# Kernel optimization log

Hardware: AMD Instinct MI355X
Metric: run time of the kernel (lower is better)

The kernel has to match this reference:

```python
import jax, jax.numpy as jnp
import numpy as np

B, C, H = 128, 3, 224
PATCH_NUM, PS = 14, 16          # patch_size = image_size / patch_num
NP = PATCH_NUM * PATCH_NUM      # 196 patches
TOP_K = 20
D = 768                         # ViT-B hidden dim
NUM_CLASSES = 1000


def setup_inputs() -> dict:
    key = jax.random.key(0)
    k1, k2, k3, k4, k5 = jax.random.split(key, 5)
    return {
        "inputs": jax.random.normal(k1, (B, C, H, H), jnp.float32),
        "patch_grad": jax.random.normal(k2, (B, NP, D), jnp.float32),
        "attack_w": jax.random.uniform(k3, (C, H, H), jnp.float32),  # torch.rand init
        "w_cls": jax.random.normal(k4, (C * NP, NUM_CLASSES), jnp.float32) * 0.02,
        "targets": jax.random.randint(k5, (B,), 0, NUM_CLASSES),
    }


def reference(inputs, patch_grad, attack_w, w_cls, targets):
    # --- top-k patch selection from patch-embedding gradients ---
    # sum over batch, then over embedding dim -> [NP]
    sum_patch = patch_grad.sum(axis=0).sum(axis=1)
    _, top_idx = jax.lax.top_k(sum_patch, TOP_K)  # distinct patch indices

    # --- vectorized equivalent of the per-pixel double loop ---
    # patch (ix, iy) -> pixel block [ix*PS:(ix+1)*PS, iy*PS:(iy+1)*PS]
    ix = top_idx // PATCH_NUM
    iy = top_idx % PATCH_NUM
    mask_p = jnp.zeros((PATCH_NUM, PATCH_NUM), inputs.dtype).at[ix, iy].set(1.0)
    mask = jnp.kron(mask_p, jnp.ones((PS, PS), inputs.dtype))  # [H, H] pixel mask
    x = inputs + mask[None, None, :, :] * attack_w[None, :, :, :]  # [B,C,H,H]

    # --- surrogate classifier head (stand-in for aux_vit second forward) ---
    # per-patch average pool, flatten, linear -> logits [B, NUM_CLASSES]
    pooled = x.reshape(B, C, PATCH_NUM, PS, PATCH_NUM, PS).mean(axis=(3, 5))
    logits = pooled.reshape(B, -1) @ w_cls

    targets_prob = jax.nn.softmax(logits, axis=1)
    # original applies CrossEntropyLoss to the *probabilities* (treats them as logits)
    logp = jax.nn.log_softmax(targets_prob, axis=1)
    ce = -jnp.take_along_axis(logp, targets[:, None], axis=1)[:, 0]  # [B]

    u = 0.0
    l2loss = jnp.mean(attack_w * attack_w)
    loss = u * l2loss - (1.0 - u) * ce.mean()
    return targets_prob, loss
```

## Files before the change

### kernel.cpp

```cpp
#include <hip/hip_runtime.h>
#include <math.h>

#define PA_OFF    0
#define APOOL_OFF 25600
#define MA_OFF    26624
#define IPOOL_OFF 28672
#define PL_OFF    106496

typedef float v4f __attribute__((ext_vector_type(4)));

__device__ __forceinline__ float hsum4(v4f v) { return (v.x + v.y) + (v.z + v.w); }

__global__ __launch_bounds__(256, 2) void k1_main(
    const float* __restrict__ inputs,
    const float* __restrict__ patch_grad,
    const float* __restrict__ attack_w,
    float* __restrict__ ws)
{
  const int bid  = blockIdx.x;
  const int lane = threadIdx.x & 63;

  if (bid < 784) {
    const int w  = bid * 4 + (threadIdx.x >> 6);
    const int R0 = w * 8;
    const v4f* src = (const v4f*)patch_grad + (size_t)R0 * 192 + lane;

    v4f v[24];
    #pragma unroll
    for (int j = 0; j < 24; ++j)
      v[j] = __builtin_nontemporal_load(src + (size_t)j * 64);
    __builtin_amdgcn_sched_barrier(0);

    float s[8];
    #pragma unroll
    for (int k = 0; k < 8; ++k)
      s[k] = hsum4(v[3 * k]) + hsum4(v[3 * k + 1]) + hsum4(v[3 * k + 2]);

    #pragma unroll
    for (int o = 32; o > 0; o >>= 1) {
      #pragma unroll
      for (int k = 0; k < 8; ++k) s[k] += __shfl_down(s[k], o, 64);
    }
    if (lane == 0) {
      float* pa = ws + PA_OFF;
      #pragma unroll
      for (int k = 0; k < 8; ++k) {
        const int row = R0 + k, b = row / 196, p = row - b * 196;
        pa[p * 128 + b] = s[k];
      }
    }
  } else {
    const int w = (bid - 784) * 4 + (threadIdx.x >> 6);
    if (w >= 5418) return;
    const int img = w / 14, px = w - img * 14;
    const float* base = (img < 384)
        ? inputs + (size_t)img * 50176
        : attack_w + (size_t)(img - 384) * 50176;
    const v4f* src = (const v4f*)(base + px * 3584);
    const int cl = (lane < 56) ? lane : 55;

    v4f v[16];
    #pragma unroll
    for (int r = 0; r < 16; ++r)
      v[r] = __builtin_nontemporal_load(src + r * 56 + cl);
    __builtin_amdgcn_sched_barrier(0);

    v4f s = v[0];
    #pragma unroll
    for (int r = 1; r < 16; ++r) s += v[r];
    s.x += __shfl_xor(s.x, 1); s.y += __shfl_xor(s.y, 1);
    s.z += __shfl_xor(s.z, 1); s.w += __shfl_xor(s.w, 1);
    s.x += __shfl_xor(s.x, 2); s.y += __shfl_xor(s.y, 2);
    s.z += __shfl_xor(s.z, 2); s.w += __shfl_xor(s.w, 2);
    if ((lane & 3) == 0 && lane < 56) {
      const int py = lane >> 2;
      const float ps = ((s.x + s.y) + (s.z + s.w)) * (1.f / 256.f);
      if (img < 384) {
        const int b = img / 3, c = img - b * 3;
        ws[IPOOL_OFF + (size_t)b * 588 + c * 196 + px * 14 + py] = ps;
      } else {
        ws[APOOL_OFF + (img - 384) * 196 + px * 14 + py] = ps;
      }
    }
  }
}

__global__ __launch_bounds__(256) void k2_topk(float* __restrict__ ws,
                                               float* __restrict__ d_loss)
{
  __shared__ float sp[196];
  __shared__ float maskp[196];
  const int t = threadIdx.x;
  if (t < 196) {
    const float4* q = (const float4*)(ws + PA_OFF + (size_t)t * 128);
    float4 a = make_float4(0.f, 0.f, 0.f, 0.f);
    #pragma unroll
    for (int j = 0; j < 32; ++j) {
      const float4 v = q[j];
      a.x += v.x; a.y += v.y; a.z += v.z; a.w += v.w;
    }
    sp[t] = (a.x + a.y) + (a.z + a.w);
  }
  if (t == 0) *d_loss = 0.f;
  __syncthreads();
  if (t < 196) {
    const float v = sp[t];
    int cnt = 0;
    for (int j = 0; j < 196; ++j) {
      const float u = sp[j];
      cnt += (u > v || (u == v && j < t)) ? 1 : 0;
    }
    maskp[t] = (cnt < 20) ? 1.f : 0.f;
  }
  __syncthreads();
  for (int k = t; k < 588; k += 256) {
    const int p = k % 196;
    ws[MA_OFF + k] = maskp[p] * ws[APOOL_OFF + k];
  }
}

__global__ __launch_bounds__(256) void k3_gemm(const float* __restrict__ w_cls,
                                               float* __restrict__ ws)
{
  __shared__ __align__(16) float lp[588 * 8];
  const int bid = blockIdx.x;
  const int nt = bid & 15;
  const int bg = bid >> 4;
  const int t  = threadIdx.x;
  const float* ipool = ws + IPOOL_OFF;
  const float* ma    = ws + MA_OFF;
  for (int idx = t; idx < 4704; idx += 256) {
    const int bb = idx / 588;
    const int kk = idx - bb * 588;
    lp[kk * 8 + bb] = ipool[(size_t)(bg * 8 + bb) * 588 + kk] + ma[kk];
  }
  __syncthreads();
  const int lane = t & 63, g = t >> 6;
  const int n = nt * 64 + lane;
  const bool valid = n < 1000;
  float a0 = 0, a1 = 0;
  const float* wc = w_cls + n;
  #pragma unroll 7
  for (int kk = 0; kk < 588; ++kk) {
    const float w = valid ? wc[(size_t)kk * 1000] : 0.f;
    const float2 pv = *(const float2*)&lp[kk * 8 + g * 2];
    a0 += pv.x * w; a1 += pv.y * w;
  }
  float* pl = ws + PL_OFF;
  const int rowb = bg * 8 + g * 2;
  pl[(size_t)(rowb + 0) * 1024 + n] = a0;
  pl[(size_t)(rowb + 1) * 1024 + n] = a1;
}

__global__ __launch_bounds__(256) void k4_softmax(const float* __restrict__ ws,
                                                  const int* __restrict__ targets,
                                                  float* __restrict__ out)
{
  __shared__ float red[4];
  __shared__ float sh_pt;
  const int b = blockIdx.x, t = threadIdx.x;
  const float* pl = ws + PL_OFF + (size_t)b * 1024;
  float l[4]; bool val[4];
  #pragma unroll
  for (int j = 0; j < 4; ++j) {
    const int n = j * 256 + t;
    val[j] = (n < 1000);
    l[j] = val[j] ? pl[n] : -INFINITY;
  }
  float m = fmaxf(fmaxf(l[0], l[1]), fmaxf(l[2], l[3]));
  #pragma unroll
  for (int o = 32; o > 0; o >>= 1) m = fmaxf(m, __shfl_down(m, o, 64));
  if ((t & 63) == 0) red[t >> 6] = m;
  __syncthreads();
  const float m1 = fmaxf(fmaxf(red[0], red[1]), fmaxf(red[2], red[3]));
  __syncthreads();
  float e[4]; float s = 0.f;
  #pragma unroll
  for (int j = 0; j < 4; ++j) { e[j] = val[j] ? expf(l[j] - m1) : 0.f; s += e[j]; }
  #pragma unroll
  for (int o = 32; o > 0; o >>= 1) s += __shfl_down(s, o, 64);
  if ((t & 63) == 0) red[t >> 6] = s;
  __syncthreads();
  const float S1 = red[0] + red[1] + red[2] + red[3];
  __syncthreads();
  const float inv = 1.f / S1;
  const int tgt = targets[b];
  float p[4];
  #pragma unroll
  for (int j = 0; j < 4; ++j) {
    const int n = j * 256 + t;
    if (val[j]) {
      p[j] = e[j] * inv;
      out[(size_t)b * 1000 + n] = p[j];
      if (n == tgt) sh_pt = p[j];
    } else {
      p[j] = -INFINITY;
    }
  }
  float m2 = fmaxf(fmaxf(p[0], p[1]), fmaxf(p[2], p[3]));
  #pragma unroll
  for (int o = 32; o > 0; o >>= 1) m2 = fmaxf(m2, __shfl_down(m2, o, 64));
  if ((t & 63) == 0) red[t >> 6] = m2;
  __syncthreads();
  const float M2 = fmaxf(fmaxf(red[0], red[1]), fmaxf(red[2], red[3]));
  __syncthreads();
  float s2 = 0.f;
  #pragma unroll
  for (int j = 0; j < 4; ++j) s2 += val[j] ? expf(p[j] - M2) : 0.f;
  #pragma unroll
  for (int o = 32; o > 0; o >>= 1) s2 += __shfl_down(s2, o, 64);
  if ((t & 63) == 0) red[t >> 6] = s2;
  __syncthreads();
  if (t == 0) {
    const float S2 = red[0] + red[1] + red[2] + red[3];
    const float lse2 = M2 + logf(S2);
    atomicAdd(out + 128000, (sh_pt - lse2) * (1.f / 128.f));
  }
}

extern "C" void kernel_launch(void* const* d_in, const int* in_sizes, int n_in,
                              void* d_out, int out_size, void* d_ws, size_t ws_size,
                              hipStream_t stream) {
  const float* inputs     = (const float*)d_in[0];
  const float* patch_grad = (const float*)d_in[1];
  const float* attack_w   = (const float*)d_in[2];
  const float* w_cls      = (const float*)d_in[3];
  const int*   targets    = (const int*)d_in[4];
  float* out = (float*)d_out;
  float* ws  = (float*)d_ws;

  hipLaunchKernelGGL(k1_main,  dim3(2139), dim3(256), 0, stream,
                     inputs, patch_grad, attack_w, ws);
  hipLaunchKernelGGL(k2_topk,  dim3(1),    dim3(256), 0, stream, ws, out + 128000);
  hipLaunchKernelGGL(k3_gemm,  dim3(256),  dim3(256), 0, stream, w_cls, ws);
  hipLaunchKernelGGL(k4_softmax, dim3(128), dim3(256), 0, stream, ws, targets, out);
}
```

Baseline: 235.7 us.

## Split classifier GEMM along K into eight partial slices reduced in softmax

The small GEMM kernel is split along the 588-long reduction dimension into 8 slices, raising the grid from 256 to 2048 blocks so more CUs are busy. Each block writes partial logits to a separate workspace slab, and the softmax kernel sums the 8 partials before proceeding. The padded shared-memory row stride also changes to 9 to reduce bank conflicts. In exchange, the workspace needs 8x more partial-logit storage, there is extra global traffic for the partials, and each block repeats the staging setup.

```diff
diff --git a/kernel.cpp b/kernel.cpp
--- a/kernel.cpp
+++ b/kernel.cpp
@@ -122,34 +122,39 @@
 __global__ __launch_bounds__(256) void k3_gemm(const float* __restrict__ w_cls,
                                                float* __restrict__ ws)
 {
-  __shared__ __align__(16) float lp[588 * 8];
+  __shared__ __align__(16) float lp[74 * 9];
   const int bid = blockIdx.x;
-  const int nt = bid & 15;
-  const int bg = bid >> 4;
+  const int ks = bid & 7;
+  const int nt = (bid >> 3) & 15;
+  const int bg = bid >> 7;
   const int t  = threadIdx.x;
+  const int kk_max = (ks == 7) ? 70 : 74;
   const float* ipool = ws + IPOOL_OFF;
   const float* ma    = ws + MA_OFF;
-  for (int idx = t; idx < 4704; idx += 256) {
-    const int bb = idx / 588;
-    const int kk = idx - bb * 588;
-    lp[kk * 8 + bb] = ipool[(size_t)(bg * 8 + bb) * 588 + kk] + ma[kk];
+  for (int idx = t; idx < 592; idx += 256) {
+    const int bb = idx & 7;
+    const int kk = idx >> 3;
+    const int k  = ks * 74 + kk;
+    lp[kk * 9 + bb] = (kk < kk_max)
+        ? ipool[(size_t)(bg * 8 + bb) * 588 + k] + ma[k]
+        : 0.f;
   }
   __syncthreads();
   const int lane = t & 63, g = t >> 6;
   const int n = nt * 64 + lane;
   const bool valid = n < 1000;
   float a0 = 0, a1 = 0;
-  const float* wc = w_cls + n;
-  #pragma unroll 7
-  for (int kk = 0; kk < 588; ++kk) {
+  const float* wc = w_cls + (size_t)ks * 74 * 1000 + n;
+  #pragma unroll 10
+  for (int kk = 0; kk < kk_max; ++kk) {
     const float w = valid ? wc[(size_t)kk * 1000] : 0.f;
-    const float2 pv = *(const float2*)&lp[kk * 8 + g * 2];
+    const float2 pv = *(const float2*)&lp[kk * 9 + g * 2];
     a0 += pv.x * w; a1 += pv.y * w;
   }
   float* pl = ws + PL_OFF;
   const int rowb = bg * 8 + g * 2;
-  pl[(size_t)(rowb + 0) * 1024 + n] = a0;
-  pl[(size_t)(rowb + 1) * 1024 + n] = a1;
+  pl[(size_t)(ks * 128 + rowb + 0) * 1024 + n] = a0;
+  pl[(size_t)(ks * 128 + rowb + 1) * 1024 + n] = a1;
 }
 
 __global__ __launch_bounds__(256) void k4_softmax(const float* __restrict__ ws,
@@ -159,13 +164,19 @@
   __shared__ float red[4];
   __shared__ float sh_pt;
   const int b = blockIdx.x, t = threadIdx.x;
-  const float* pl = ws + PL_OFF + (size_t)b * 1024;
+  const float* pl = ws + PL_OFF;
   float l[4]; bool val[4];
   #pragma unroll
   for (int j = 0; j < 4; ++j) {
     const int n = j * 256 + t;
     val[j] = (n < 1000);
-    l[j] = val[j] ? pl[n] : -INFINITY;
+    float s = -INFINITY;
+    if (val[j]) {
+      s = 0.f;
+      #pragma unroll
+      for (int ks = 0; ks < 8; ++ks) s += pl[(size_t)(ks * 128 + b) * 1024 + n];
+    }
+    l[j] = s;
   }
   float m = fmaxf(fmaxf(l[0], l[1]), fmaxf(l[2], l[3]));
   #pragma unroll
@@ -232,6 +243,6 @@
   hipLaunchKernelGGL(k1_main,  dim3(2139), dim3(256), 0, stream,
                      inputs, patch_grad, attack_w, ws);
   hipLaunchKernelGGL(k2_topk,  dim3(1),    dim3(256), 0, stream, ws, out + 128000);
-  hipLaunchKernelGGL(k3_gemm,  dim3(256),  dim3(256), 0, stream, w_cls, ws);
+  hipLaunchKernelGGL(k3_gemm,  dim3(2048), dim3(256), 0, stream, w_cls, ws);
   hipLaunchKernelGGL(k4_softmax, dim3(128), dim3(256), 0, stream, ws, targets, out);
 }
```

After: 189.3 us, median of 2. -19.7%, faster.
